# Optimization experiments

Hardware: AMD Instinct MI355X
Metric: run time of the kernel (lower is better)

The kernel has to match this reference:

```python
import jax, jax.numpy as jnp
import numpy as np

C = 64
D = C // 8  # query/key channels
B, H, W = 4, 64, 64


def setup_inputs() -> dict:
    key = jax.random.key(0)
    ks = jax.random.split(key, 8)
    x = jax.random.normal(ks[0], (B, C, H, W), dtype=jnp.float32)
    # 1x1 conv params (kernel squeezed to [out_ch, in_ch])
    sq = 1.0 / np.sqrt(C)
    Wq = jax.random.uniform(ks[1], (D, C), jnp.float32, -sq, sq)
    bq = jax.random.uniform(ks[2], (D,), jnp.float32, -sq, sq)
    Wk = jax.random.uniform(ks[3], (D, C), jnp.float32, -sq, sq)
    bk = jax.random.uniform(ks[4], (D,), jnp.float32, -sq, sq)
    Wv = jax.random.uniform(ks[5], (C, C), jnp.float32, -sq, sq)
    bv = jax.random.uniform(ks[6], (C,), jnp.float32, -sq, sq)
    # gamma is zero-initialized in the module; use a nonzero value so the
    # attention path actually contributes to the output.
    gamma = jax.random.normal(ks[7], (1,), dtype=jnp.float32)
    return {"x": x, "Wq": Wq, "bq": bq, "Wk": Wk, "bk": bk, "Wv": Wv, "bv": bv, "gamma": gamma}


def reference(x, Wq, bq, Wk, bk, Wv, bv, gamma):
    b, c, h, w = x.shape
    n = h * w
    xf = x.reshape(b, c, n)                                   # [B,C,N]
    q = jnp.einsum('dc,bcn->bdn', Wq, xf) + bq[None, :, None]  # [B,D,N]
    k = jnp.einsum('dc,bcn->bdn', Wk, xf) + bk[None, :, None]  # [B,D,N]
    v = jnp.einsum('ec,bcn->ben', Wv, xf) + bv[None, :, None]  # [B,C,N]
    energy = jnp.einsum('bdn,bdm->bnm', q, k)                  # [B,N,N] = Q^T K
    attn = jax.nn.softmax(energy, axis=-1)                     # softmax over keys m
    # out[b,c,n] = sum_m v[b,c,m] * attn[b,n,m]  (V @ attention^T in torch)
    out = jnp.einsum('bcm,bnm->bcn', v, attn).reshape(b, c, h, w)
    return gamma[0] * out + x
```

## Files before the change

### kernel.cpp

```cpp
#include <hip/hip_runtime.h>
#include <hip/hip_bf16.h>
#include <math.h>

#define BB 4
#define CC 64
#define DD 8
#define NN 4096
#define KS 8
#define KPS (NN / KS)
#define LOG2E 1.44269504088896340736f

typedef __attribute__((ext_vector_type(4))) short short4v;
typedef __attribute__((ext_vector_type(8))) unsigned short ushort8;
typedef __attribute__((ext_vector_type(16))) float f32x16;

#if defined(__HIP_DEVICE_COMPILE__)
  #if __has_builtin(__builtin_amdgcn_mfma_f32_32x32x8bf16_1k)
    #define MFMA32x8(A, B, C) __builtin_amdgcn_mfma_f32_32x32x8bf16_1k(A, B, C, 0, 0, 0)
  #elif __has_builtin(__builtin_amdgcn_mfma_f32_32x32x8_bf16)
    #define MFMA32x8(A, B, C) __builtin_amdgcn_mfma_f32_32x32x8_bf16(A, B, C, 0, 0, 0)
  #else
    #error "no 32x32x8 bf16 MFMA builtin in device pass"
  #endif
#else
  static __device__ __host__ inline f32x16 MFMA32x8(short4v, short4v, f32x16 c) { return c; }
#endif

static __device__ inline short4v pack4(float a, float b, float c, float d) {
    union { short4v s; __hip_bfloat162 h[2]; } u;
    u.h[0] = __float22bfloat162_rn(make_float2(a, b));
    u.h[1] = __float22bfloat162_rn(make_float2(c, d));
    return u.s;
}

__global__ __launch_bounds__(256) void qkv_kernel(
    const float* __restrict__ x,  const float* __restrict__ Wq, const float* __restrict__ bq,
    const float* __restrict__ Wk, const float* __restrict__ bk,
    const float* __restrict__ Wv, const float* __restrict__ bv,
    unsigned short* __restrict__ qb, unsigned short* __restrict__ kb,
    unsigned short* __restrict__ vT)
{
    __shared__ unsigned short LQ[128 * 8];
    __shared__ unsigned short LK[128 * 8];

    int tid = threadIdx.x;
    int wave = tid >> 6, lane = tid & 63;
    int l32 = lane & 31, h2 = lane >> 5;

    int blk = blockIdx.x;
    int b = blk & (BB - 1);
    int r2 = blk >> 2;
    int rt = r2 % 3;
    int ng = r2 / 3;
    int n0 = ng * 128 + wave * 32;

    short4v af[8];
    #pragma unroll
    for (int s = 0; s < 8; ++s) {
        float4 w4;
        if (rt < 2) {
            w4 = *(const float4*)(Wv + (size_t)(rt * 32 + l32) * CC + s * 8 + 4 * h2);
        } else if (l32 < 8) {
            w4 = *(const float4*)(Wq + (size_t)l32 * CC + s * 8 + 4 * h2);
        } else if (l32 < 16) {
            w4 = *(const float4*)(Wk + (size_t)(l32 - 8) * CC + s * 8 + 4 * h2);
        } else {
            w4 = make_float4(0.f, 0.f, 0.f, 0.f);
        }
        af[s] = pack4(w4.x, w4.y, w4.z, w4.w);
    }

    const float* xb = x + (size_t)b * CC * NN + n0 + l32;
    short4v bf[8];
    #pragma unroll
    for (int s = 0; s < 8; ++s) {
        int c0 = s * 8 + 4 * h2;
        float x0 = xb[(size_t)(c0 + 0) * NN];
        float x1 = xb[(size_t)(c0 + 1) * NN];
        float x2 = xb[(size_t)(c0 + 2) * NN];
        float x3 = xb[(size_t)(c0 + 3) * NN];
        bf[s] = pack4(x0, x1, x2, x3);
    }

    f32x16 acc;
    #pragma unroll
    for (int r = 0; r < 16; ++r) acc[r] = 0.f;
    #pragma unroll
    for (int s = 0; s < 8; ++s)
        acc = MFMA32x8(af[s], bf[s], acc);

    if (rt < 2) {
        #pragma unroll
        for (int r = 0; r < 16; ++r) {
            int row = rt * 32 + (r & 3) + 8 * (r >> 2) + 4 * h2;
            float val = acc[r] + bv[row];
            __hip_bfloat16 hv = __float2bfloat16(val);
            vT[((size_t)b * CC + row) * NN + n0 + l32] = *(unsigned short*)&hv;
        }
    } else {
        short4v qp = pack4((acc[0] + bq[0 + 4 * h2]) * LOG2E,
                           (acc[1] + bq[1 + 4 * h2]) * LOG2E,
                           (acc[2] + bq[2 + 4 * h2]) * LOG2E,
                           (acc[3] + bq[3 + 4 * h2]) * LOG2E);
        short4v kp = pack4(acc[4] + bk[0 + 4 * h2],
                           acc[5] + bk[1 + 4 * h2],
                           acc[6] + bk[2 + 4 * h2],
                           acc[7] + bk[3 + 4 * h2]);
        int nl = wave * 32 + l32;
        *(short4v*)(LQ + (size_t)nl * 8 + 4 * h2) = qp;
        *(short4v*)(LK + (size_t)nl * 8 + 4 * h2) = kp;
        __syncthreads();
        if (tid < 128) {
            ushort8 row = *(const ushort8*)(LQ + (size_t)tid * 8);
            *(ushort8*)(qb + ((size_t)b * NN + ng * 128 + tid) * 8) = row;
        } else {
            int t = tid - 128;
            ushort8 row = *(const ushort8*)(LK + (size_t)t * 8);
            *(ushort8*)(kb + ((size_t)b * NN + ng * 128 + t) * 8) = row;
        }
    }
}

__global__ __launch_bounds__(256, 4) void flash_kernel(
    const unsigned short* __restrict__ qb, const unsigned short* __restrict__ kb,
    const unsigned short* __restrict__ vT, unsigned short* __restrict__ accb,
    float* __restrict__ sbuf)
{
    __shared__ unsigned short VS[64 * 132];
    int tid = threadIdx.x;
    int wave = tid >> 6, lane = tid & 63;
    int l32 = lane & 31, h2 = lane >> 5;

    int blk = blockIdx.x;
    int b = blk & (BB - 1);
    int rest = blk >> 2;
    int split = rest & (KS - 1);
    int qchunk = rest >> 3;
    int n0 = qchunk * 128 + wave * 32;

    short4v qf = *(const short4v*)(qb + ((size_t)b * NN + n0 + l32) * DD + h2 * 4);

    const unsigned short* kbb = kb + (size_t)b * NN * DD;
    const unsigned short* vbb = vT + (size_t)b * CC * NN;
    int m0 = split * KPS;

    int cch = tid >> 4, kg = tid & 15;
    int kgx = (kg ^ (cch & 3)) * 8;

    f32x16 o0, o1, zz;
    #pragma unroll
    for (int r = 0; r < 16; ++r) { o0[r] = 0.f; o1[r] = 0.f; zz[r] = 0.f; }
    float ssum = 0.f;

    ushort8 vr0 = *(const ushort8*)(vbb + (size_t)(cch)      * NN + m0 + kg * 8);
    ushort8 vr1 = *(const ushort8*)(vbb + (size_t)(16 + cch) * NN + m0 + kg * 8);
    ushort8 vr2 = *(const ushort8*)(vbb + (size_t)(32 + cch) * NN + m0 + kg * 8);
    ushort8 vr3 = *(const ushort8*)(vbb + (size_t)(48 + cch) * NN + m0 + kg * 8);

    for (int tile = 0; tile < 4; ++tile) {
        *(ushort8*)(VS + (size_t)(cch)      * 132 + kgx) = vr0;
        *(ushort8*)(VS + (size_t)(16 + cch) * 132 + kgx) = vr1;
        *(ushort8*)(VS + (size_t)(32 + cch) * 132 + kgx) = vr2;
        *(ushort8*)(VS + (size_t)(48 + cch) * 132 + kgx) = vr3;
        __syncthreads();

        if (tile < 3) {
            int mn = m0 + (tile + 1) * 128;
            vr0 = *(const ushort8*)(vbb + (size_t)(cch)      * NN + mn + kg * 8);
            vr1 = *(const ushort8*)(vbb + (size_t)(16 + cch) * NN + mn + kg * 8);
            vr2 = *(const ushort8*)(vbb + (size_t)(32 + cch) * NN + mn + kg * 8);
            vr3 = *(const ushort8*)(vbb + (size_t)(48 + cch) * NN + mn + kg * 8);
        }

        short4v kf[4];
        #pragma unroll
        for (int s = 0; s < 4; ++s)
            kf[s] = *(const short4v*)(kbb + (size_t)(m0 + tile * 128 + s * 32 + l32) * DD + h2 * 4);

        #pragma unroll
        for (int sub = 0; sub < 4; ++sub) {
            f32x16 st = MFMA32x8(kf[sub], qf, zz);
            float w[16];
            #pragma unroll
            for (int r = 0; r < 16; ++r) w[r] = exp2f(st[r]);
            ssum += (((w[0] + w[1]) + (w[2] + w[3])) + ((w[4] + w[5]) + (w[6] + w[7])))
                  + (((w[8] + w[9]) + (w[10] + w[11])) + ((w[12] + w[13]) + (w[14] + w[15])));

            union { short4v s; __hip_bfloat162 h[2]; } u[4];
            #pragma unroll
            for (int g = 0; g < 4; ++g) {
                u[g].h[0] = __float22bfloat162_rn(make_float2(w[4 * g],     w[4 * g + 1]));
                u[g].h[1] = __float22bfloat162_rn(make_float2(w[4 * g + 2], w[4 * g + 3]));
            }
            #pragma unroll
            for (int g = 0; g < 4; ++g) {
                int go = ((sub * 4 + g) ^ (l32 & 3)) * 8 + h2 * 4;
                short4v vf0 = *(const short4v*)(VS + (size_t)(l32)      * 132 + go);
                short4v vf1 = *(const short4v*)(VS + (size_t)(32 + l32) * 132 + go);
                o0 = MFMA32x8(u[g].s, vf0, o0);
                o1 = MFMA32x8(u[g].s, vf1, o1);
            }
        }
        __syncthreads();
    }

    __hip_bfloat16* ab = (__hip_bfloat16*)accb + (((size_t)(b * KS + split)) * NN + n0) * CC;
    #pragma unroll
    for (int r = 0; r < 16; ++r) {
        int qrow = (r & 3) + 8 * (r >> 2) + 4 * h2;
        ab[(size_t)qrow * CC + l32]      = __float2bfloat16(o0[r]);
        ab[(size_t)qrow * CC + 32 + l32] = __float2bfloat16(o1[r]);
    }
    ssum += __shfl_xor(ssum, 32);
    if (lane < 32)
        sbuf[(size_t)(b * KS + split) * NN + n0 + l32] = ssum;
}

__global__ __launch_bounds__(256) void merge_kernel(
    const unsigned short* __restrict__ accb, const float* __restrict__ sbuf,
    const float* __restrict__ x, const float* __restrict__ gamma,
    float* __restrict__ out)
{
    __shared__ float tile[16 * 65];
    __shared__ float stl[16];
    int blk = blockIdx.x;
    int b = blk >> 8;
    int n0 = (blk & 255) * 16;
    int tid = threadIdx.x;

    if (tid < 16) {
        float st = 0.f;
        #pragma unroll
        for (int sp = 0; sp < KS; ++sp)
            st += sbuf[(size_t)(b * KS + sp) * NN + n0 + tid];
        stl[tid] = 1.0f / st;
    }
    const __hip_bfloat16* ac = (const __hip_bfloat16*)accb;
    #pragma unroll
    for (int p = 0; p < 4; ++p) {
        int e = p * 256 + tid;
        int c = e & 63, nl = e >> 6;
        float a = 0.f;
        #pragma unroll
        for (int sp = 0; sp < KS; ++sp)
            a += __bfloat162float(ac[(((size_t)(b * KS + sp) * NN) + n0 + nl) * CC + c]);
        tile[nl * 65 + c] = a;
    }
    __syncthreads();
    float g = gamma[0];
    #pragma unroll
    for (int p = 0; p < 4; ++p) {
        int e = p * 256 + tid;
        int nl = e & 15, c = e >> 4;
        size_t xi = ((size_t)b * CC + c) * NN + n0 + nl;
        out[xi] = g * tile[nl * 65 + c] * stl[nl] + x[xi];
    }
}

extern "C" void kernel_launch(void* const* d_in, const int* in_sizes, int n_in,
                              void* d_out, int out_size, void* d_ws, size_t ws_size,
                              hipStream_t stream)
{
    const float* x     = (const float*)d_in[0];
    const float* Wq    = (const float*)d_in[1];
    const float* bq    = (const float*)d_in[2];
    const float* Wk    = (const float*)d_in[3];
    const float* bk    = (const float*)d_in[4];
    const float* Wv    = (const float*)d_in[5];
    const float* bv    = (const float*)d_in[6];
    const float* gamma = (const float*)d_in[7];
    float* out = (float*)d_out;

    float* ws = (float*)d_ws;
    size_t off = 0;
    unsigned short* qb = (unsigned short*)(ws + off); off += (size_t)BB * NN * DD / 2 + 64;
    unsigned short* kb = (unsigned short*)(ws + off); off += (size_t)BB * NN * DD / 2 + 64;
    unsigned short* vT = (unsigned short*)(ws + off); off += (size_t)BB * CC * NN / 2 + 64;
    unsigned short* accb = (unsigned short*)(ws + off); off += (size_t)BB * KS * NN * CC / 2;
    float* sbuf = ws + off; off += (size_t)BB * KS * NN;

    qkv_kernel<<<BB * 3 * 32, 256, 0, stream>>>(x, Wq, bq, Wk, bk, Wv, bv, qb, kb, vT);
    flash_kernel<<<BB * (NN / 128) * KS, 256, 0, stream>>>(qb, kb, vT, accb, sbuf);
    merge_kernel<<<BB * 256, 256, 0, stream>>>(accb, sbuf, x, gamma, out);
}
```

Baseline: 106.3 us.

## Reduce split-K partials with float atomics instead of bf16 partial buffers

The flash kernel now accumulates its per-split output and row sums straight into a single fp32 buffer using unsafeAtomicAdd, instead of writing eight bf16 partial slices for a separate merge pass to sum. A memset zeroes the buffer first, and a lighter norm kernel only divides by the row sum and adds the residual. Smaller changes replace exp2f with the hardware exp2 builtin and split the row-sum accumulator into four chains. The aim is to cut merge traffic, at the cost of atomic contention, an extra memset launch and a non-deterministic summation order.

```diff
diff --git a/kernel.cpp b/kernel.cpp
--- a/kernel.cpp
+++ b/kernel.cpp
@@ -22,8 +22,14 @@
   #else
     #error "no 32x32x8 bf16 MFMA builtin in device pass"
   #endif
+  #if __has_builtin(__builtin_amdgcn_exp2f)
+    #define EXP2(x) __builtin_amdgcn_exp2f(x)
+  #else
+    #define EXP2(x) exp2f(x)
+  #endif
 #else
   static __device__ __host__ inline f32x16 MFMA32x8(short4v, short4v, f32x16 c) { return c; }
+  #define EXP2(x) exp2f(x)
 #endif
 
 static __device__ inline short4v pack4(float a, float b, float c, float d) {
@@ -123,8 +129,8 @@
 
 __global__ __launch_bounds__(256, 4) void flash_kernel(
     const unsigned short* __restrict__ qb, const unsigned short* __restrict__ kb,
-    const unsigned short* __restrict__ vT, unsigned short* __restrict__ accb,
-    float* __restrict__ sbuf)
+    const unsigned short* __restrict__ vT, float* __restrict__ obuf,
+    float* __restrict__ ssb)
 {
     __shared__ unsigned short VS[64 * 132];
     int tid = threadIdx.x;
@@ -150,7 +156,7 @@
     f32x16 o0, o1, zz;
     #pragma unroll
     for (int r = 0; r < 16; ++r) { o0[r] = 0.f; o1[r] = 0.f; zz[r] = 0.f; }
-    float ssum = 0.f;
+    float s0 = 0.f, s1 = 0.f, s2 = 0.f, s3 = 0.f;
 
     ushort8 vr0 = *(const ushort8*)(vbb + (size_t)(cch)      * NN + m0 + kg * 8);
     ushort8 vr1 = *(const ushort8*)(vbb + (size_t)(16 + cch) * NN + m0 + kg * 8);
@@ -182,9 +188,11 @@
             f32x16 st = MFMA32x8(kf[sub], qf, zz);
             float w[16];
             #pragma unroll
-            for (int r = 0; r < 16; ++r) w[r] = exp2f(st[r]);
-            ssum += (((w[0] + w[1]) + (w[2] + w[3])) + ((w[4] + w[5]) + (w[6] + w[7])))
-                  + (((w[8] + w[9]) + (w[10] + w[11])) + ((w[12] + w[13]) + (w[14] + w[15])));
+            for (int r = 0; r < 16; ++r) w[r] = EXP2(st[r]);
+            s0 += (w[0] + w[1]) + (w[2] + w[3]);
+            s1 += (w[4] + w[5]) + (w[6] + w[7]);
+            s2 += (w[8] + w[9]) + (w[10] + w[11]);
+            s3 += (w[12] + w[13]) + (w[14] + w[15]);
 
             union { short4v s; __hip_bfloat162 h[2]; } u[4];
             #pragma unroll
@@ -204,56 +212,51 @@
         __syncthreads();
     }
 
-    __hip_bfloat16* ab = (__hip_bfloat16*)accb + (((size_t)(b * KS + split)) * NN + n0) * CC;
+    float* ob = obuf + ((size_t)(b * NN + n0)) * CC;
     #pragma unroll
     for (int r = 0; r < 16; ++r) {
         int qrow = (r & 3) + 8 * (r >> 2) + 4 * h2;
-        ab[(size_t)qrow * CC + l32]      = __float2bfloat16(o0[r]);
-        ab[(size_t)qrow * CC + 32 + l32] = __float2bfloat16(o1[r]);
-    }
+        unsafeAtomicAdd(ob + (size_t)qrow * CC + l32,      o0[r]);
+        unsafeAtomicAdd(ob + (size_t)qrow * CC + 32 + l32, o1[r]);
+    }
+    float ssum = (s0 + s1) + (s2 + s3);
     ssum += __shfl_xor(ssum, 32);
     if (lane < 32)
-        sbuf[(size_t)(b * KS + split) * NN + n0 + l32] = ssum;
-}
-
-__global__ __launch_bounds__(256) void merge_kernel(
-    const unsigned short* __restrict__ accb, const float* __restrict__ sbuf,
+        unsafeAtomicAdd(ssb + (size_t)b * NN + n0 + l32, ssum);
+}
+
+__global__ __launch_bounds__(256) void norm_kernel(
+    const float* __restrict__ obuf, const float* __restrict__ ssb,
     const float* __restrict__ x, const float* __restrict__ gamma,
     float* __restrict__ out)
 {
-    __shared__ float tile[16 * 65];
-    __shared__ float stl[16];
+    __shared__ float tile[32 * 65];
+    __shared__ float stl[32];
     int blk = blockIdx.x;
-    int b = blk >> 8;
-    int n0 = (blk & 255) * 16;
+    int b = blk >> 7;
+    int n0 = (blk & 127) * 32;
     int tid = threadIdx.x;
 
-    if (tid < 16) {
-        float st = 0.f;
-        #pragma unroll
-        for (int sp = 0; sp < KS; ++sp)
-            st += sbuf[(size_t)(b * KS + sp) * NN + n0 + tid];
-        stl[tid] = 1.0f / st;
-    }
-    const __hip_bfloat16* ac = (const __hip_bfloat16*)accb;
-    #pragma unroll
-    for (int p = 0; p < 4; ++p) {
-        int e = p * 256 + tid;
-        int c = e & 63, nl = e >> 6;
-        float a = 0.f;
-        #pragma unroll
-        for (int sp = 0; sp < KS; ++sp)
-            a += __bfloat162float(ac[(((size_t)(b * KS + sp) * NN) + n0 + nl) * CC + c]);
-        tile[nl * 65 + c] = a;
+    if (tid < 32) stl[tid] = 1.0f / ssb[(size_t)b * NN + n0 + tid];
+
+    int nl = tid >> 4, cg = tid & 15;
+    #pragma unroll
+    for (int p = 0; p < 2; ++p) {
+        int n = p * 16 + nl;
+        float4 v = *(const float4*)(obuf + ((size_t)(b * NN + n0 + n)) * CC + cg * 4);
+        tile[n * 65 + cg * 4 + 0] = v.x;
+        tile[n * 65 + cg * 4 + 1] = v.y;
+        tile[n * 65 + cg * 4 + 2] = v.z;
+        tile[n * 65 + cg * 4 + 3] = v.w;
     }
     __syncthreads();
     float g = gamma[0];
     #pragma unroll
-    for (int p = 0; p < 4; ++p) {
-        int e = p * 256 + tid;
-        int nl = e & 15, c = e >> 4;
-        size_t xi = ((size_t)b * CC + c) * NN + n0 + nl;
-        out[xi] = g * tile[nl * 65 + c] * stl[nl] + x[xi];
+    for (int p = 0; p < 8; ++p) {
+        int idx = p * 256 + tid;
+        int c = idx >> 5, n_l = idx & 31;
+        size_t xi = ((size_t)b * CC + c) * NN + n0 + n_l;
+        out[xi] = g * tile[n_l * 65 + c] * stl[n_l] + x[xi];
     }
 }
 
@@ -276,10 +279,12 @@
     unsigned short* qb = (unsigned short*)(ws + off); off += (size_t)BB * NN * DD / 2 + 64;
     unsigned short* kb = (unsigned short*)(ws + off); off += (size_t)BB * NN * DD / 2 + 64;
     unsigned short* vT = (unsigned short*)(ws + off); off += (size_t)BB * CC * NN / 2 + 64;
-    unsigned short* accb = (unsigned short*)(ws + off); off += (size_t)BB * KS * NN * CC / 2;
-    float* sbuf = ws + off; off += (size_t)BB * KS * NN;
+    float* obuf = ws + off; off += (size_t)BB * NN * CC;
+    float* ssb  = ws + off; off += (size_t)BB * NN;
+
+    hipMemsetAsync(obuf, 0, ((size_t)BB * NN * CC + (size_t)BB * NN) * sizeof(float), stream);
 
     qkv_kernel<<<BB * 3 * 32, 256, 0, stream>>>(x, Wq, bq, Wk, bk, Wv, bv, qb, kb, vT);
-    flash_kernel<<<BB * (NN / 128) * KS, 256, 0, stream>>>(qb, kb, vT, accb, sbuf);
-    merge_kernel<<<BB * 256, 256, 0, stream>>>(accb, sbuf, x, gamma, out);
-}
+    flash_kernel<<<BB * (NN / 128) * KS, 256, 0, stream>>>(qb, kb, vT, obuf, ssb);
+    norm_kernel<<<BB * 128, 256, 0, stream>>>(obuf, ssb, x, gamma, out);
+}
```

Result: slower. 114.8 us (+8.1%).
